# Optimization experiments

Measured on AMD Instinct MI355X. Metric: run time of the kernel, lower is better.

Reference implementation:

```python
import jax, jax.numpy as jnp
import numpy as np

B = 4096        # number of motif graphs in the batch
H = 256         # hidden_channels
P = 128         # num_prototypes
V = 2000        # motif vocab size (embedding table has V+1 rows)
N_ATOMS = 32768 # focal context atoms
N_RES = 262144  # residues
KNN = 4         # construct_num_neighbors (and cos_sim topk)
DIST_TH = 6.0


def setup_inputs() -> dict:
    key = jax.random.key(0)
    ks = jax.random.split(key, 14)
    return {
        "h_ctx_focal": jax.random.normal(ks[0], (N_ATOMS, H), jnp.float32),
        "pos_ctx_focal": jax.random.normal(ks[1], (N_ATOMS, 3), jnp.float32) * 5.0,
        "h_residue": jax.random.normal(ks[2], (N_RES, H), jnp.float32),
        "residue_pos": jax.random.normal(ks[3], (N_RES, 3, 3), jnp.float32) * 3.0,
        "embedding_weight": jax.random.normal(ks[4], (V + 1, H), jnp.float32) * 0.02,
        "prototypes": jax.random.normal(ks[5], (P, H), jnp.float32),
        "prototype_count": jax.random.uniform(ks[6], (P, V), jnp.float32) * 10.0,
        "motif_w": jax.random.normal(ks[7], (3 * H, H), jnp.float32) * 0.02,
        "motif_b": jnp.zeros((H,), jnp.float32),
        "gnn_w1": jax.random.normal(ks[8], (H, H), jnp.float32) * 0.05,
        "gnn_w2": jax.random.normal(ks[9], (H, H), jnp.float32) * 0.05,
        "current_wid": jax.random.randint(ks[10], (B,), 0, V),
        "current_atoms_batch": jnp.sort(jax.random.randint(ks[11], (N_ATOMS,), 0, B)),
        "amino_acid_batch": jnp.sort(jax.random.randint(ks[12], (N_RES,), 0, B)),
    }


def _l2norm(x, axis=-1):
    # F.normalize: x / max(||x||, eps)
    n = jnp.linalg.norm(x, axis=axis, keepdims=True)
    return x / jnp.maximum(n, 1e-12)


def reference(h_ctx_focal, pos_ctx_focal, h_residue, residue_pos,
              embedding_weight, prototypes, prototype_count,
              motif_w, motif_b, gnn_w1, gnn_w2,
              current_wid, current_atoms_batch, amino_acid_batch):
    # --- scatter-based motif aggregation (forward_motif) ---
    node_hiddens = jax.ops.segment_sum(h_ctx_focal, current_atoms_batch, num_segments=B)
    motif_hiddens = embedding_weight[current_wid]                       # [B,H]
    pos_sum = jax.ops.segment_sum(pos_ctx_focal, current_atoms_batch, num_segments=B)
    cnt = jax.ops.segment_sum(jnp.ones((N_ATOMS,), pos_ctx_focal.dtype),
                              current_atoms_batch, num_segments=B)
    center_pos = pos_sum / jnp.maximum(cnt, 1.0)[:, None]               # scatter_mean [B,3]

    # distance-thresholded residue gather-reduce (CA atom = index 1)
    ca = residue_pos[:, 1, :]                                           # [N_RES,3]
    dist = jnp.linalg.norm(ca - center_pos[amino_acid_batch], axis=1)
    rmask = (dist < DIST_TH).astype(h_residue.dtype)                    # [N_RES]
    residue_emb = jax.ops.segment_sum(h_residue * rmask[:, None],
                                      amino_acid_batch, num_segments=B)  # [B,H]

    # --- MGraph.output: prototype kNN graph + prototype->motif tf-idf edges ---
    cos = _l2norm(residue_emb) @ _l2norm(prototypes).T                  # [B,P]
    _, knn_idx = jax.lax.top_k(cos, KNN)                                # [B,KNN]
    dim = B + P + V
    adj = jnp.zeros((dim, dim), residue_emb.dtype)
    ind1 = knn_idx.T.reshape(-1) + B
    ind0 = jnp.tile(jnp.arange(B), KNN)
    adj = adj.at[ind0, ind1].set(1.0)
    sum_proto = jnp.sum(prototype_count, axis=1, keepdims=True)         # [P,1]
    sum_motif = jnp.sum((prototype_count > 0).astype(jnp.float32), axis=0)  # [V]
    block = prototype_count / (sum_proto + 1.0) * (
        jnp.log((1.0 + P) / (1.0 + sum_motif)) + 1.0)                   # [P,V]
    adj = adj.at[B:B + P, B + P:].set(block)
    A = adj + adj.T  # edge duplication with swapped indices == symmetrize

    # --- WeightGNN (2-layer weighted message passing over the motif graph) ---
    node_feat = jnp.concatenate([residue_emb, prototypes, embedding_weight[:V]], axis=0)
    h1 = jax.nn.relu((A @ node_feat) @ gnn_w1)
    residue_out = ((A @ h1) @ gnn_w2)[:B]                               # [B,H]

    # --- prediction head ---
    pred_vecs = jnp.concatenate([0.8 * node_hiddens,
                                 0.7 * motif_hiddens,
                                 1.5 * residue_out], axis=-1)           # [B,3H]
    pred_scores = (pred_vecs @ motif_w + motif_b) @ embedding_weight.T  # [B,V+1]
    return pred_scores
```

## Files before the change

### kernel.cpp

```cpp
#include <hip/hip_runtime.h>
#include <hip/hip_bf16.h>
#include <math.h>

#define NB 4096
#define HD 256
#define NP 128
#define NV 2000
#define NATOMS 32768
#define NRES 262144
#define VCHUNK 125

typedef __attribute__((ext_vector_type(8))) short bf16x8;
typedef __attribute__((ext_vector_type(4))) float f32x4;
typedef __attribute__((ext_vector_type(8))) unsigned short u16x8;

__device__ __forceinline__ unsigned short f2bf(float f) {
  unsigned int u = __builtin_bit_cast(unsigned int, f);
  u += 0x7FFFu + ((u >> 16) & 1u);
  return (unsigned short)(u >> 16);
}
__device__ __forceinline__ float bf2f(unsigned short h) {
  unsigned int u = ((unsigned int)h) << 16;
  return __builtin_bit_cast(float, u);
}

__device__ __forceinline__ int lower_bound_i(const int* __restrict__ arr, int n, int val) {
  int lo = 0, hi = n;
  while (lo < hi) { int mid = (lo + hi) >> 1; if (arr[mid] < val) lo = mid + 1; else hi = mid; }
  return lo;
}

#define E_ATOMS 4096
#define E_SP    (E_ATOMS + 128)
#define E_WL    (E_SP + 8)
#define E_PR    (E_WL + 128)
#define E_HZ    (E_PR + 128)
#define E_ES    (E_HZ + 512)
#define E_MS    (E_ES + 192)

__global__ __launch_bounds__(256) void k_init(
    const float* __restrict__ hctx, const float* __restrict__ pos, const int* __restrict__ ab,
    const float* __restrict__ pcnt, const float* __restrict__ proto,
    const float* __restrict__ emb, const float* __restrict__ mw,
    float* __restrict__ nh, float* __restrict__ center, float* __restrict__ inv_sp,
    float* __restrict__ wl, float* __restrict__ pnT, float* __restrict__ hin,
    unsigned short* __restrict__ embH, unsigned short* __restrict__ embL,
    unsigned short* __restrict__ mwTH, unsigned short* __restrict__ mwTL) {
  int blk = blockIdx.x, t = threadIdx.x;
  __shared__ float red[256];
  if (blk < E_ATOMS) {
    int b = blk;
    int s = lower_bound_i(ab, NATOMS, b);
    int e = lower_bound_i(ab, NATOMS, b + 1);
    float a0 = 0.f, a1 = 0.f, a2 = 0.f, a3 = 0.f;
    int a = s;
    for (; a + 3 < e; a += 4) {
      a0 += hctx[(size_t)(a + 0) * HD + t];
      a1 += hctx[(size_t)(a + 1) * HD + t];
      a2 += hctx[(size_t)(a + 2) * HD + t];
      a3 += hctx[(size_t)(a + 3) * HD + t];
    }
    for (; a < e; ++a) a0 += hctx[(size_t)a * HD + t];
    nh[(size_t)b * HD + t] = (a0 + a1) + (a2 + a3);
    if (t < 3) {
      float ps = 0.f;
      for (int aa = s; aa < e; ++aa) ps += pos[aa * 3 + t];
      center[b * 3 + t] = ps / fmaxf((float)(e - s), 1.0f);
    }
  } else if (blk < E_SP) {
    int p = blk - E_ATOMS;
    float s = 0.f;
    for (int v = t; v < NV; v += 256) s += pcnt[(size_t)p * NV + v];
    red[t] = s; __syncthreads();
    for (int off = 128; off; off >>= 1) { if (t < off) red[t] += red[t + off]; __syncthreads(); }
    if (!t) inv_sp[p] = 1.0f / (red[0] + 1.0f);
  } else if (blk < E_WL) {
    int v = (blk - E_SP) * 256 + t;
    if (v < NV) {
      float sm = 0.f;
      for (int p = 0; p < NP; ++p) sm += (pcnt[(size_t)p * NV + v] > 0.f) ? 1.f : 0.f;
      wl[v] = logf((1.0f + NP) / (1.0f + sm)) + 1.0f;
    }
  } else if (blk < E_PR) {
    int p = blk - E_WL;
    float x = proto[p * HD + t];
    red[t] = x * x; __syncthreads();
    for (int off = 128; off; off >>= 1) { if (t < off) red[t] += red[t + off]; __syncthreads(); }
    float inv = 1.0f / fmaxf(sqrtf(red[0]), 1e-12f);
    pnT[t * NP + p] = x * inv;
  } else if (blk < E_HZ) {
    hin[(blk - E_PR) * 256 + t] = 0.f;
  } else if (blk < E_ES) {
    int e0 = ((blk - E_HZ) * 256 + t) * 4;
#pragma unroll
    for (int j = 0; j < 4; ++j) {
      int e = e0 + j;
      if (e < 2001 * HD) {
        float x = emb[e];
        unsigned short h = f2bf(x);
        embH[e] = h; embL[e] = f2bf(x - bf2f(h));
      } else {
        embH[e] = 0; embL[e] = 0;
      }
    }
  } else {
    int e0 = ((blk - E_ES) * 256 + t) * 4;
#pragma unroll
    for (int j = 0; j < 4; ++j) {
      int e = e0 + j;
      int n = e / 768, k = e - n * 768;
      float x = mw[(size_t)k * HD + n];
      unsigned short h = f2bf(x);
      mwTH[e] = h; mwTL[e] = f2bf(x - bf2f(h));
    }
  }
}

__global__ __launch_bounds__(256) void k_res_topk_bemb(
    const float* __restrict__ hres, const float* __restrict__ rpos,
    const int* __restrict__ rb, const float* __restrict__ center,
    const float* __restrict__ pcnt, const float* __restrict__ wl,
    const float* __restrict__ inv_sp, const float* __restrict__ emb,
    const float* __restrict__ pnT, int* __restrict__ knn, float* __restrict__ hin) {
  int blk = blockIdx.x, t = threadIdx.x;
  __shared__ int lst[256];
  __shared__ int cnt;
  __shared__ float cw[VCHUNK];
  __shared__ float sre[HD];
  __shared__ float part[256];
  __shared__ float c[NP];
  __shared__ float rv[256];
  __shared__ int ri[256];
  __shared__ int kk[4];
  if (blk < NB) {
    int b = blk;
    int s = lower_bound_i(rb, NRES, b);
    int e = lower_bound_i(rb, NRES, b + 1);
    float c0 = center[b * 3], c1 = center[b * 3 + 1], c2 = center[b * 3 + 2];
    float a0 = 0.f, a1 = 0.f, a2 = 0.f, a3 = 0.f, a4 = 0.f, a5 = 0.f, a6 = 0.f, a7 = 0.f;
    for (int cc = s; cc < e; cc += 256) {
      if (!t) cnt = 0;
      __syncthreads();
      int r = cc + t;
      if (r < e) {
        float dx = rpos[(size_t)r * 9 + 3] - c0;
        float dy = rpos[(size_t)r * 9 + 4] - c1;
        float dz = rpos[(size_t)r * 9 + 5] - c2;
        if (dx * dx + dy * dy + dz * dz < 36.0f) {
          int j = atomicAdd(&cnt, 1);
          lst[j] = r;
        }
      }
      __syncthreads();
      int n = cnt;
      int j = 0;
      for (; j + 7 < n; j += 8) {
        a0 += hres[(size_t)lst[j + 0] * HD + t];
        a1 += hres[(size_t)lst[j + 1] * HD + t];
        a2 += hres[(size_t)lst[j + 2] * HD + t];
        a3 += hres[(size_t)lst[j + 3] * HD + t];
        a4 += hres[(size_t)lst[j + 4] * HD + t];
        a5 += hres[(size_t)lst[j + 5] * HD + t];
        a6 += hres[(size_t)lst[j + 6] * HD + t];
        a7 += hres[(size_t)lst[j + 7] * HD + t];
      }
      for (; j < n; ++j) a0 += hres[(size_t)lst[j] * HD + t];
      __syncthreads();
    }
    float acc = ((a0 + a1) + (a2 + a3)) + ((a4 + a5) + (a6 + a7));
    sre[t] = acc;
    part[t] = acc * acc;
    __syncthreads();
    for (int off = 128; off; off >>= 1) { if (t < off) part[t] += part[t + off]; __syncthreads(); }
    float invn = 1.0f / fmaxf(sqrtf(part[0]), 1e-12f);
    __syncthreads();
    int p = t & 127, half = t >> 7;
    float d = 0.f;
    int h0 = half * 128;
#pragma unroll 8
    for (int h = h0; h < h0 + 128; ++h) d += sre[h] * pnT[h * NP + p];
    part[t] = d;
    __syncthreads();
    if (t < NP) c[t] = (part[t] + part[t + 128]) * invn;
    __syncthreads();
    for (int k = 0; k < 4; ++k) {
      rv[t] = (t < NP) ? c[t] : -INFINITY;
      ri[t] = t;
      __syncthreads();
      for (int off = 128; off; off >>= 1) {
        if (t < off) {
          float ov = rv[t + off]; int oi = ri[t + off];
          if (ov > rv[t] || (ov == rv[t] && oi < ri[t])) { rv[t] = ov; ri[t] = oi; }
        }
        __syncthreads();
      }
      if (!t) { knn[b * 4 + k] = ri[0]; kk[k] = ri[0]; }
      if (t == ri[0]) c[t] = -INFINITY;
      __syncthreads();
    }
#pragma unroll
    for (int k = 0; k < 4; ++k) atomicAdd(&hin[kk[k] * HD + t], sre[t]);
  } else {
    int pc = blk - NB;
    int p = pc >> 4, ch = pc & 15;
    int v0 = ch * VCHUNK;
    float isp = inv_sp[p];
    for (int v = t; v < VCHUNK; v += 256) cw[v] = pcnt[(size_t)p * NV + v0 + v] * wl[v0 + v] * isp;
    __syncthreads();
    float acc = 0.f;
#pragma unroll 8
    for (int v = 0; v < VCHUNK; ++v) acc += cw[v] * emb[(size_t)(v0 + v) * HD + t];
    atomicAdd(&hin[p * HD + t], acc);
  }
}

__global__ __launch_bounds__(256) void k_h1hw(const float* __restrict__ hin,
                                              const float* __restrict__ w1,
                                              const float* __restrict__ w2,
                                              float* __restrict__ hw) {
  int p = blockIdx.x, t = threadIdx.x;
  __shared__ float s[HD], s2[HD];
  s[t] = hin[p * HD + t];
  __syncthreads();
  float a = 0.f;
#pragma unroll 8
  for (int h = 0; h < HD; ++h) a += s[h] * w1[h * HD + t];
  s2[t] = fmaxf(a, 0.f);
  __syncthreads();
  float o = 0.f;
#pragma unroll 8
  for (int h = 0; h < HD; ++h) o += s2[h] * w2[h * HD + t];
  hw[p * HD + t] = o;
}

__global__ __launch_bounds__(512) void k_gemm1(
    const float* __restrict__ nh, const float* __restrict__ emb,
    const int* __restrict__ wid, const int* __restrict__ knn, const float* __restrict__ hw,
    const unsigned short* __restrict__ mwTH, const unsigned short* __restrict__ mwTL,
    const float* __restrict__ mb,
    unsigned short* __restrict__ tbH, unsigned short* __restrict__ tbL) {
  __shared__ __align__(16) unsigned short Ah[64][40], Al[64][40], Bh[64][40], Bl[64][40];
  __shared__ int swid[64];
  __shared__ int4 sknn[64];
  int tid = threadIdx.x, lane = tid & 63, w = tid >> 6;
  int wm = (w & 1) * 32, wn = (w >> 1) * 16;
  int bm = blockIdx.x * 64, bn = blockIdx.y * 64;
  if (tid < 64) { swid[tid] = wid[bm + tid]; sknn[tid] = ((const int4*)knn)[bm + tid]; }
  f32x4 acc[2] = {};
  for (int k0 = 0; k0 < 768; k0 += 32) {
    __syncthreads();
    for (int i = tid; i < 2048; i += 512) {
      int m = i >> 5, k = i & 31;
      float x;
      if (k0 < 256) {
        x = 0.8f * nh[(size_t)(bm + m) * HD + k0 + k];
      } else if (k0 < 512) {
        x = 0.7f * emb[(size_t)swid[m] * HD + (k0 - 256) + k];
      } else {
        int4 kn = sknn[m];
        int kk2 = (k0 - 512) + k;
        x = 1.5f * (hw[kn.x * HD + kk2] + hw[kn.y * HD + kk2] +
                    hw[kn.z * HD + kk2] + hw[kn.w * HD + kk2]);
      }
      unsigned short h = f2bf(x);
      Ah[m][k] = h; Al[m][k] = f2bf(x - bf2f(h));
    }
    if (tid < 256) {
      int e = tid * 8, n = e >> 5, k = e & 31;
      size_t idx = (size_t)(bn + n) * 768 + k0 + k;
      *(u16x8*)&Bh[n][k] = *(const u16x8*)&mwTH[idx];
      *(u16x8*)&Bl[n][k] = *(const u16x8*)&mwTL[idx];
    }
    __syncthreads();
    int r = lane & 15, kb = (lane >> 4) * 8;
    bf16x8 bh = *(const bf16x8*)&Bh[wn + r][kb];
    bf16x8 bl = *(const bf16x8*)&Bl[wn + r][kb];
#pragma unroll
    for (int i = 0; i < 2; ++i) {
      bf16x8 ah = *(const bf16x8*)&Ah[wm + i * 16 + r][kb];
      bf16x8 al = *(const bf16x8*)&Al[wm + i * 16 + r][kb];
      acc[i] = __builtin_amdgcn_mfma_f32_16x16x32_bf16(ah, bh, acc[i], 0, 0, 0);
      acc[i] = __builtin_amdgcn_mfma_f32_16x16x32_bf16(ah, bl, acc[i], 0, 0, 0);
      acc[i] = __builtin_amdgcn_mfma_f32_16x16x32_bf16(al, bh, acc[i], 0, 0, 0);
    }
  }
  int col0 = lane & 15, row0 = (lane >> 4) * 4;
  int col = bn + wn + col0;
  float bv = mb[col];
#pragma unroll
  for (int i = 0; i < 2; ++i)
#pragma unroll
    for (int rr = 0; rr < 4; ++rr) {
      int row = bm + wm + i * 16 + row0 + rr;
      float x = acc[i][rr] + bv;
      unsigned short h = f2bf(x);
      tbH[(size_t)row * HD + col] = h;
      tbL[(size_t)row * HD + col] = f2bf(x - bf2f(h));
    }
}

__global__ __launch_bounds__(256) void k_gemm2(
    const unsigned short* __restrict__ tbH, const unsigned short* __restrict__ tbL,
    const unsigned short* __restrict__ embH, const unsigned short* __restrict__ embL,
    float* __restrict__ out) {
  __shared__ __align__(16) unsigned short AH[128][40], AL[128][40], BH[128][40], BL[128][40];
  int tid = threadIdx.x, lane = tid & 63, w = tid >> 6;
  int wm = (w & 1) * 64, wn = (w >> 1) * 64;
  int bm = blockIdx.x * 128, bn = blockIdx.y * 128;
  f32x4 acc[4][4] = {};
  for (int k0 = 0; k0 < HD; k0 += 32) {
    __syncthreads();
#pragma unroll
    for (int cch = 0; cch < 2; ++cch) {
      int e = (tid + cch * 256) * 8;
      int m = e >> 5, k = e & 31;
      *(u16x8*)&AH[m][k] = *(const u16x8*)&tbH[(size_t)(bm + m) * HD + k0 + k];
      *(u16x8*)&AL[m][k] = *(const u16x8*)&tbL[(size_t)(bm + m) * HD + k0 + k];
      *(u16x8*)&BH[m][k] = *(const u16x8*)&embH[(size_t)(bn + m) * HD + k0 + k];
      *(u16x8*)&BL[m][k] = *(const u16x8*)&embL[(size_t)(bn + m) * HD + k0 + k];
    }
    __syncthreads();
    int r = lane & 15, kb = (lane >> 4) * 8;
    bf16x8 ah[4], al[4], bh[4], bl[4];
#pragma unroll
    for (int i = 0; i < 4; ++i) {
      ah[i] = *(const bf16x8*)&AH[wm + i * 16 + r][kb];
      al[i] = *(const bf16x8*)&AL[wm + i * 16 + r][kb];
      bh[i] = *(const bf16x8*)&BH[wn + i * 16 + r][kb];
      bl[i] = *(const bf16x8*)&BL[wn + i * 16 + r][kb];
    }
#pragma unroll
    for (int i = 0; i < 4; ++i)
#pragma unroll
      for (int j = 0; j < 4; ++j) {
        acc[i][j] = __builtin_amdgcn_mfma_f32_16x16x32_bf16(ah[i], bh[j], acc[i][j], 0, 0, 0);
        acc[i][j] = __builtin_amdgcn_mfma_f32_16x16x32_bf16(ah[i], bl[j], acc[i][j], 0, 0, 0);
        acc[i][j] = __builtin_amdgcn_mfma_f32_16x16x32_bf16(al[i], bh[j], acc[i][j], 0, 0, 0);
      }
  }
  int col0 = lane & 15, row0 = (lane >> 4) * 4;
#pragma unroll
  for (int i = 0; i < 4; ++i)
#pragma unroll
    for (int j = 0; j < 4; ++j) {
      int col = bn + wn + j * 16 + col0;
      if (col <= 2000) {
#pragma unroll
        for (int rr = 0; rr < 4; ++rr) {
          int row = bm + wm + i * 16 + row0 + rr;
          out[(size_t)row * 2001 + col] = acc[i][j][rr];
        }
      }
    }
}

extern "C" void kernel_launch(void* const* d_in, const int* in_sizes, int n_in,
                              void* d_out, int out_size, void* d_ws, size_t ws_size,
                              hipStream_t stream) {
  const float* hctx  = (const float*)d_in[0];
  const float* pos   = (const float*)d_in[1];
  const float* hres  = (const float*)d_in[2];
  const float* rpos  = (const float*)d_in[3];
  const float* emb   = (const float*)d_in[4];
  const float* proto = (const float*)d_in[5];
  const float* pcnt  = (const float*)d_in[6];
  const float* mw    = (const float*)d_in[7];
  const float* mb    = (const float*)d_in[8];
  const float* w1    = (const float*)d_in[9];
  const float* w2    = (const float*)d_in[10];
  const int* wid     = (const int*)d_in[11];
  const int* ab      = (const int*)d_in[12];
  const int* rb      = (const int*)d_in[13];
  float* out = (float*)d_out;

  float* ws     = (float*)d_ws;
  float* nh     = ws;
  float* center = nh + (size_t)NB * HD;
  float* inv_sp = center + (size_t)NB * 4;
  float* wl     = inv_sp + 128;
  float* pnT    = wl + 2048;
  float* hin    = pnT + NP * HD;
  float* hw     = hin + NP * HD;
  int*   knn    = (int*)(hw + NP * HD);
  unsigned short* tbH  = (unsigned short*)(knn + NB * 4);
  unsigned short* tbL  = tbH + (size_t)NB * HD;
  unsigned short* embH = tbL + (size_t)NB * HD;
  unsigned short* embL = embH + (size_t)2048 * HD;
  unsigned short* mwTH = embL + (size_t)2048 * HD;
  unsigned short* mwTL = mwTH + (size_t)768 * HD;

  k_init<<<E_MS, 256, 0, stream>>>(hctx, pos, ab, pcnt, proto, emb, mw,
                                   nh, center, inv_sp, wl, pnT, hin,
                                   embH, embL, mwTH, mwTL);
  k_res_topk_bemb<<<NB + NP * 16, 256, 0, stream>>>(hres, rpos, rb, center,
                                                    pcnt, wl, inv_sp, emb, pnT, knn, hin);
  k_h1hw<<<NP, 256, 0, stream>>>(hin, w1, w2, hw);
  k_gemm1<<<dim3(NB / 64, 4), 512, 0, stream>>>(nh, emb, wid, knn, hw,
                                                mwTH, mwTL, mb, tbH, tbL);
  k_gemm2<<<dim3(NB / 128, 16), 256, 0, stream>>>(tbH, tbL, embH, embL, out);
}
```

Before: 548.5 us.

## Fuse atom segment-sum into residue kernel, precompute segment starts, swizzle gemm2 grid

Builds segment start tables for atoms and residues in the init kernel from sorted batch arrays, replacing the per-block binary searches. Moves the atom feature and position segment sums into the residue-filtering kernel so the center is kept in shared memory instead of round-tripping through a global buffer. The output GEMM now uses a 1D grid with a block-index swizzle to improve L2 reuse of the tile operands. Fusing adds serial atom work ahead of the residue scan in each block, and the start tables rely on the batch arrays being sorted.

```diff
diff --git a/kernel.cpp b/kernel.cpp
--- a/kernel.cpp
+++ b/kernel.cpp
@@ -24,74 +24,51 @@
   return __builtin_bit_cast(float, u);
 }
 
-__device__ __forceinline__ int lower_bound_i(const int* __restrict__ arr, int n, int val) {
-  int lo = 0, hi = n;
-  while (lo < hi) { int mid = (lo + hi) >> 1; if (arr[mid] < val) lo = mid + 1; else hi = mid; }
-  return lo;
-}
-
-#define E_ATOMS 4096
-#define E_SP    (E_ATOMS + 128)
-#define E_WL    (E_SP + 8)
-#define E_PR    (E_WL + 128)
-#define E_HZ    (E_PR + 128)
-#define E_ES    (E_HZ + 512)
-#define E_MS    (E_ES + 192)
-
-__global__ __launch_bounds__(256) void k_init(
-    const float* __restrict__ hctx, const float* __restrict__ pos, const int* __restrict__ ab,
+#define I_SP   128
+#define I_WL   (I_SP + 8)
+#define I_PR   (I_WL + 128)
+#define I_HZ   (I_PR + 128)
+#define I_ES   (I_HZ + 512)
+#define I_MS   (I_ES + 192)
+#define I_AS   (I_MS + 128)
+#define I_RS   (I_AS + 1024)
+
+__global__ __launch_bounds__(256) void k_init0(
+    const int* __restrict__ ab, const int* __restrict__ rb,
     const float* __restrict__ pcnt, const float* __restrict__ proto,
     const float* __restrict__ emb, const float* __restrict__ mw,
-    float* __restrict__ nh, float* __restrict__ center, float* __restrict__ inv_sp,
-    float* __restrict__ wl, float* __restrict__ pnT, float* __restrict__ hin,
+    float* __restrict__ inv_sp, float* __restrict__ wl, float* __restrict__ pnT,
+    float* __restrict__ hin,
     unsigned short* __restrict__ embH, unsigned short* __restrict__ embL,
-    unsigned short* __restrict__ mwTH, unsigned short* __restrict__ mwTL) {
+    unsigned short* __restrict__ mwTH, unsigned short* __restrict__ mwTL,
+    int* __restrict__ astart, int* __restrict__ rstart) {
   int blk = blockIdx.x, t = threadIdx.x;
   __shared__ float red[256];
-  if (blk < E_ATOMS) {
-    int b = blk;
-    int s = lower_bound_i(ab, NATOMS, b);
-    int e = lower_bound_i(ab, NATOMS, b + 1);
-    float a0 = 0.f, a1 = 0.f, a2 = 0.f, a3 = 0.f;
-    int a = s;
-    for (; a + 3 < e; a += 4) {
-      a0 += hctx[(size_t)(a + 0) * HD + t];
-      a1 += hctx[(size_t)(a + 1) * HD + t];
-      a2 += hctx[(size_t)(a + 2) * HD + t];
-      a3 += hctx[(size_t)(a + 3) * HD + t];
-    }
-    for (; a < e; ++a) a0 += hctx[(size_t)a * HD + t];
-    nh[(size_t)b * HD + t] = (a0 + a1) + (a2 + a3);
-    if (t < 3) {
-      float ps = 0.f;
-      for (int aa = s; aa < e; ++aa) ps += pos[aa * 3 + t];
-      center[b * 3 + t] = ps / fmaxf((float)(e - s), 1.0f);
-    }
-  } else if (blk < E_SP) {
-    int p = blk - E_ATOMS;
+  if (blk < I_SP) {
+    int p = blk;
     float s = 0.f;
     for (int v = t; v < NV; v += 256) s += pcnt[(size_t)p * NV + v];
     red[t] = s; __syncthreads();
     for (int off = 128; off; off >>= 1) { if (t < off) red[t] += red[t + off]; __syncthreads(); }
     if (!t) inv_sp[p] = 1.0f / (red[0] + 1.0f);
-  } else if (blk < E_WL) {
-    int v = (blk - E_SP) * 256 + t;
+  } else if (blk < I_WL) {
+    int v = (blk - I_SP) * 256 + t;
     if (v < NV) {
       float sm = 0.f;
       for (int p = 0; p < NP; ++p) sm += (pcnt[(size_t)p * NV + v] > 0.f) ? 1.f : 0.f;
       wl[v] = logf((1.0f + NP) / (1.0f + sm)) + 1.0f;
     }
-  } else if (blk < E_PR) {
-    int p = blk - E_WL;
+  } else if (blk < I_PR) {
+    int p = blk - I_WL;
     float x = proto[p * HD + t];
     red[t] = x * x; __syncthreads();
     for (int off = 128; off; off >>= 1) { if (t < off) red[t] += red[t + off]; __syncthreads(); }
     float inv = 1.0f / fmaxf(sqrtf(red[0]), 1e-12f);
     pnT[t * NP + p] = x * inv;
-  } else if (blk < E_HZ) {
-    hin[(blk - E_PR) * 256 + t] = 0.f;
-  } else if (blk < E_ES) {
-    int e0 = ((blk - E_HZ) * 256 + t) * 4;
+  } else if (blk < I_HZ) {
+    hin[(blk - I_PR) * 256 + t] = 0.f;
+  } else if (blk < I_ES) {
+    int e0 = ((blk - I_HZ) * 256 + t) * 4;
 #pragma unroll
     for (int j = 0; j < 4; ++j) {
       int e = e0 + j;
@@ -103,8 +80,8 @@
         embH[e] = 0; embL[e] = 0;
       }
     }
-  } else {
-    int e0 = ((blk - E_ES) * 256 + t) * 4;
+  } else if (blk < I_MS) {
+    int e0 = ((blk - I_ES) * 256 + t) * 4;
 #pragma unroll
     for (int j = 0; j < 4; ++j) {
       int e = e0 + j;
@@ -113,15 +90,31 @@
       unsigned short h = f2bf(x);
       mwTH[e] = h; mwTL[e] = f2bf(x - bf2f(h));
     }
+  } else if (blk < I_AS) {
+    int i = (blk - I_MS) * 256 + t;
+    int cur = ab[i];
+    int prev = (i == 0) ? -1 : ab[i - 1];
+    for (int b = prev + 1; b <= cur; ++b) astart[b] = i;
+    if (i == NATOMS - 1)
+      for (int b = cur + 1; b <= NB; ++b) astart[b] = NATOMS;
+  } else {
+    int i = (blk - I_AS) * 256 + t;
+    int cur = rb[i];
+    int prev = (i == 0) ? -1 : rb[i - 1];
+    for (int b = prev + 1; b <= cur; ++b) rstart[b] = i;
+    if (i == NRES - 1)
+      for (int b = cur + 1; b <= NB; ++b) rstart[b] = NRES;
   }
 }
 
-__global__ __launch_bounds__(256) void k_res_topk_bemb(
+__global__ __launch_bounds__(256) void k_mega(
+    const float* __restrict__ hctx, const float* __restrict__ pos,
     const float* __restrict__ hres, const float* __restrict__ rpos,
-    const int* __restrict__ rb, const float* __restrict__ center,
+    const int* __restrict__ astart, const int* __restrict__ rstart,
     const float* __restrict__ pcnt, const float* __restrict__ wl,
     const float* __restrict__ inv_sp, const float* __restrict__ emb,
-    const float* __restrict__ pnT, int* __restrict__ knn, float* __restrict__ hin) {
+    const float* __restrict__ pnT,
+    float* __restrict__ nh, int* __restrict__ knn, float* __restrict__ hin) {
   int blk = blockIdx.x, t = threadIdx.x;
   __shared__ int lst[256];
   __shared__ int cnt;
@@ -132,17 +125,36 @@
   __shared__ float rv[256];
   __shared__ int ri[256];
   __shared__ int kk[4];
+  __shared__ float scen[3];
   if (blk < NB) {
     int b = blk;
-    int s = lower_bound_i(rb, NRES, b);
-    int e = lower_bound_i(rb, NRES, b + 1);
-    float c0 = center[b * 3], c1 = center[b * 3 + 1], c2 = center[b * 3 + 2];
+    int s = astart[b], e = astart[b + 1];
+    {
+      float a0 = 0.f, a1 = 0.f, a2 = 0.f, a3 = 0.f;
+      int a = s;
+      for (; a + 3 < e; a += 4) {
+        a0 += hctx[(size_t)(a + 0) * HD + t];
+        a1 += hctx[(size_t)(a + 1) * HD + t];
+        a2 += hctx[(size_t)(a + 2) * HD + t];
+        a3 += hctx[(size_t)(a + 3) * HD + t];
+      }
+      for (; a < e; ++a) a0 += hctx[(size_t)a * HD + t];
+      nh[(size_t)b * HD + t] = (a0 + a1) + (a2 + a3);
+      if (t < 3) {
+        float ps = 0.f;
+        for (int aa = s; aa < e; ++aa) ps += pos[aa * 3 + t];
+        scen[t] = ps / fmaxf((float)(e - s), 1.0f);
+      }
+    }
+    __syncthreads();
+    float c0 = scen[0], c1 = scen[1], c2 = scen[2];
+    int rs = rstart[b], re_ = rstart[b + 1];
     float a0 = 0.f, a1 = 0.f, a2 = 0.f, a3 = 0.f, a4 = 0.f, a5 = 0.f, a6 = 0.f, a7 = 0.f;
-    for (int cc = s; cc < e; cc += 256) {
+    for (int cc = rs; cc < re_; cc += 256) {
       if (!t) cnt = 0;
       __syncthreads();
       int r = cc + t;
-      if (r < e) {
+      if (r < re_) {
         float dx = rpos[(size_t)r * 9 + 3] - c0;
         float dy = rpos[(size_t)r * 9 + 4] - c1;
         float dz = rpos[(size_t)r * 9 + 5] - c2;
@@ -306,7 +318,9 @@
   __shared__ __align__(16) unsigned short AH[128][40], AL[128][40], BH[128][40], BL[128][40];
   int tid = threadIdx.x, lane = tid & 63, w = tid >> 6;
   int wm = (w & 1) * 64, wn = (w >> 1) * 64;
-  int bm = blockIdx.x * 128, bn = blockIdx.y * 128;
+  int orig = blockIdx.x;
+  int swz = (orig & 7) * 64 + (orig >> 3);
+  int bm = (swz & 31) * 128, bn = (swz >> 5) * 128;
   f32x4 acc[4][4] = {};
   for (int k0 = 0; k0 < HD; k0 += 32) {
     __syncthreads();
@@ -375,27 +389,28 @@
 
   float* ws     = (float*)d_ws;
   float* nh     = ws;
-  float* center = nh + (size_t)NB * HD;
-  float* inv_sp = center + (size_t)NB * 4;
+  float* inv_sp = nh + (size_t)NB * HD;
   float* wl     = inv_sp + 128;
   float* pnT    = wl + 2048;
   float* hin    = pnT + NP * HD;
   float* hw     = hin + NP * HD;
   int*   knn    = (int*)(hw + NP * HD);
-  unsigned short* tbH  = (unsigned short*)(knn + NB * 4);
+  int*   astart = knn + NB * 4;
+  int*   rstart = astart + 4104;
+  unsigned short* tbH  = (unsigned short*)(rstart + 4104);
   unsigned short* tbL  = tbH + (size_t)NB * HD;
   unsigned short* embH = tbL + (size_t)NB * HD;
   unsigned short* embL = embH + (size_t)2048 * HD;
   unsigned short* mwTH = embL + (size_t)2048 * HD;
   unsigned short* mwTL = mwTH + (size_t)768 * HD;
 
-  k_init<<<E_MS, 256, 0, stream>>>(hctx, pos, ab, pcnt, proto, emb, mw,
-                                   nh, center, inv_sp, wl, pnT, hin,
-                                   embH, embL, mwTH, mwTL);
-  k_res_topk_bemb<<<NB + NP * 16, 256, 0, stream>>>(hres, rpos, rb, center,
-                                                    pcnt, wl, inv_sp, emb, pnT, knn, hin);
+  k_init0<<<I_RS, 256, 0, stream>>>(ab, rb, pcnt, proto, emb, mw,
+                                    inv_sp, wl, pnT, hin,
+                                    embH, embL, mwTH, mwTL, astart, rstart);
+  k_mega<<<NB + NP * 16, 256, 0, stream>>>(hctx, pos, hres, rpos, astart, rstart,
+                                           pcnt, wl, inv_sp, emb, pnT, nh, knn, hin);
   k_h1hw<<<NP, 256, 0, stream>>>(hin, w1, w2, hw);
   k_gemm1<<<dim3(NB / 64, 4), 512, 0, stream>>>(nh, emb, wid, knn, hw,
                                                 mwTH, mwTL, mb, tbH, tbL);
-  k_gemm2<<<dim3(NB / 128, 16), 256, 0, stream>>>(tbH, tbL, embH, embL, out);
-}
+  k_gemm2<<<512, 256, 0, stream>>>(tbH, tbL, embH, embL, out);
+}
```

Measured after the change: 534.9 us. 1.03x faster.
